# Optimization experiments

Measured on AMD Instinct MI355X. Metric: run time of the kernel, lower is better.

Reference implementation:

```python
import jax, jax.numpy as jnp
import numpy as np

ML_R_PRIORI = 1.5   # mainlobe_window_radius_priori
ML_R_MAX = 4        # mainlobe_window_radius_max
MIN_K = 1           # min_k
ML_WIDTH_POW = 1    # ml_width_pow
DIST_SENTINEL = 100.0


def _grid_offsets(r):
    # all (dy, dx) pairs in [-r, r]^2 -> [(2r+1)^2, 2]
    o = np.arange(-r, r + 1)
    yy, xx = np.meshgrid(o, o, indexing='ij')
    return np.stack([yy.ravel(), xx.ravel()], axis=-1).astype(np.int32)


def setup_inputs() -> dict:
    key = jax.random.key(0)
    B, C, H, W = 256, 324, 18, 18
    k1, k2 = jax.random.split(key)
    cost_volume = jax.random.normal(k1, (B, C, H, W), dtype=jnp.float32)
    peak_coords = jax.random.randint(k2, (B, C, 2), 0, H, dtype=jnp.int32)  # (y, x)
    gy, gx = jnp.meshgrid(jnp.arange(H, dtype=jnp.int32),
                          jnp.arange(W, dtype=jnp.int32), indexing='ij')
    mesh_y = jnp.broadcast_to(gy, (B, C, H, W))
    mesh_x = jnp.broadcast_to(gx, (B, C, H, W))
    return {"cost_volume": cost_volume, "peak_coords": peak_coords,
            "mesh_y": mesh_y, "mesh_x": mesh_x}


def reference(cost_volume, peak_coords, mesh_y, mesh_x):
    B, C, H, W = cost_volume.shape
    BC, HW = B * C, H * W
    cv = cost_volume.reshape(BC, HW)
    peak = peak_coords.reshape(BC, 2)
    my = mesh_y.reshape(BC, HW)
    mx = mesh_x.reshape(BC, HW)

    # --- static offset tables ---
    off_max = jnp.asarray(_grid_offsets(ML_R_MAX))                     # [81, 2]
    off_p = jnp.asarray(_grid_offsets(int(np.ceil(ML_R_PRIORI))))      # [25, 2]
    norm_p = jnp.sqrt(jnp.sum(off_p.astype(jnp.float32) ** 2, -1))
    off_priori = jnp.where((norm_p <= ML_R_PRIORI)[:, None], off_p, 0)  # out-of-radius -> (0,0)

    bidx = jnp.arange(BC)[:, None]

    def scatter_zero_mask(offsets):
        # offsets: [1 or BC, N, 2]; zero out mainlobe window around each peak
        win = peak[:, None, :] + offsets
        wy = jnp.clip(win[..., 0], 0, H - 1)
        wx = jnp.clip(win[..., 1], 0, W - 1)
        flat = wy * W + wx                                  # [BC, N]
        return jnp.ones((BC, HW), jnp.float32).at[bidx, flat].set(0.0)

    # --- priori sidelobe mean ---
    w_pri = scatter_zero_mask(off_priori[None])
    n_pri = w_pri.sum(-1, keepdims=True)
    mean_pri = (cv * w_pri).sum(-1, keepdims=True) / n_pri

    # --- distance to nearest below-mean (sidelobe) point -> mainlobe width ---
    py, px = peak[:, :1], peak[:, 1:]
    dist = jnp.sqrt(((my - py) ** 2 + (mx - px) ** 2).astype(jnp.float32))
    pos = jnp.arange(HW, dtype=jnp.int32)[None]
    peak_flat = py * W + px
    keep = (cv <= mean_pri) & (pos != peak_flat)
    dist = jnp.where(keep, dist, DIST_SENTINEL)
    neg_small, _ = jax.lax.top_k(-dist, MIN_K)              # k smallest distances
    width = (-neg_small).mean(-1, keepdims=True)            # [BC, 1]

    # --- data-dependent mainlobe window (per-row radius) ---
    radius = jnp.clip(width, 1.5, ML_R_MAX + 0.5)           # [BC, 1]
    norms_max = jnp.sqrt(jnp.sum(off_max.astype(jnp.float32) ** 2, -1))  # [81]
    in_r = norms_max[None, :] <= radius                     # [BC, 81]
    off_dyn = jnp.where(in_r[..., None], off_max[None], 0)  # [BC, 81, 2]

    w = scatter_zero_mask(off_dyn)
    n = w.sum(-1, keepdims=True)
    mean_s = (cv * w).sum(-1, keepdims=True) / n
    var_s = (((cv - mean_s) * w) ** 2).sum(-1, keepdims=True) / (n - 1.0)  # use_std_dev=False
    peaks = cv.max(-1, keepdims=True)

    psrw = ((peaks - mean_s) / (var_s * width ** ML_WIDTH_POW + 1e-16)).reshape(B, C)
    saliency = psrw / (psrw.mean(-1, keepdims=True) + 1e-8)
    return saliency
```

## Files before the change

### kernel.cpp

```cpp
#include <hip/hip_runtime.h>
#include <math.h>

constexpr int Hn = 18, Wn = 18, HWn = 324;

__global__ __launch_bounds__(256) void psrw_kernel(
    const float* __restrict__ cv, const int* __restrict__ peak,
    float* __restrict__ out, int BC)
{
    int gtid = blockIdx.x * 256 + threadIdx.x;
    int wave = gtid >> 6;
    int lane = threadIdx.x & 63;
    int g = lane >> 4;
    int l = lane & 15;
    int tile = wave * 4 + g;
    if (tile >= BC) return;

    const float* row = cv + (size_t)tile * HWn;
    int2 pk = ((const int2*)peak)[tile];
    int py = pk.x, px = pk.y;

    const float4* rf4 = (const float4*)row;
    float4 v0 = rf4[l];
    float4 v1 = rf4[l + 16];
    float4 v2 = rf4[l + 32];
    float4 v3 = rf4[l + 48];
    float4 v4 = rf4[l + 64];
    float tl = row[320 + (l & 3)];
    bool valid20 = (l < 4);

    float c[21] = {v0.x, v0.y, v0.z, v0.w, v1.x, v1.y, v1.z, v1.w,
                   v2.x, v2.y, v2.z, v2.w, v3.x, v3.y, v3.z, v3.w,
                   v4.x, v4.y, v4.z, v4.w, valid20 ? tl : 0.f};
    int d2[21];

    float m = -INFINITY, s_pri = 0.f;
    int l4 = 4 * l;
#pragma unroll
    for (int j = 0; j < 21; ++j) {
        int p = (j < 20) ? (l4 + 64 * (j >> 2) + (j & 3)) : (320 + (l & 3));
        int y = (p * 57) >> 10;
        int x = p - 18 * y;
        int dy = y - py, dx = x - px;
        int dd = dy * dy + dx * dx;
        if (j == 20) dd = valid20 ? dd : (1 << 20);
        d2[j] = dd;
        m = fmaxf(m, (j == 20 && !valid20) ? -INFINITY : c[j]);
        s_pri += (dd > 2) ? c[j] : 0.f;
    }
#pragma unroll
    for (int o = 8; o; o >>= 1) {
        s_pri += __shfl_xor(s_pri, o, 64);
        m = fmaxf(m, __shfl_xor(m, o, 64));
    }
    int rh = min(Hn - 1, py + 1) - max(0, py - 1) + 1;
    int rw = min(Wn - 1, px + 1) - max(0, px - 1) + 1;
    int n_pri = HWn - rh * rw;
    float mean_pri = s_pri / (float)n_pri;

    int dmin = 1 << 20;
#pragma unroll
    for (int j = 0; j < 21; ++j) {
        bool keep = (c[j] <= mean_pri) && (d2[j] != 0);
        dmin = min(dmin, keep ? d2[j] : (1 << 20));
    }
#pragma unroll
    for (int o = 8; o; o >>= 1) dmin = min(dmin, __shfl_xor(dmin, o, 64));

    float width = (dmin >= (1 << 20)) ? 100.f : sqrtf((float)dmin);
    int rad2 = (dmin <= 2) ? 2 : ((dmin >= 21) ? 20 : dmin);

    float s_dyn = 0.f, ss_dyn = 0.f;
    int cnt_in = 0;
#pragma unroll
    for (int j = 0; j < 21; ++j) {
        bool in = (d2[j] <= rad2);
        float cm = in ? 0.f : c[j];
        s_dyn += cm;
        ss_dyn = fmaf(cm, cm, ss_dyn);
        cnt_in += in ? 1 : 0;
    }
#pragma unroll
    for (int o = 8; o; o >>= 1) {
        s_dyn  += __shfl_xor(s_dyn, o, 64);
        ss_dyn += __shfl_xor(ss_dyn, o, 64);
        cnt_in += __shfl_xor(cnt_in, o, 64);
    }
    float n = (float)(HWn - cnt_in);
    float mean_s = s_dyn / n;
    float var_s = fmaf(-s_dyn, mean_s, ss_dyn) / (n - 1.f);
    float psrw = (m - mean_s) / fmaf(var_s, width, 1e-16f);
    if (l == 0) out[tile] = psrw;
}

__global__ __launch_bounds__(256) void norm_kernel(float* __restrict__ out, int B)
{
    int gtid = blockIdx.x * 256 + threadIdx.x;
    int wave = gtid >> 6;
    int lane = threadIdx.x & 63;
    if (wave >= B) return;
    float* row = out + (size_t)wave * HWn;
    float4 v0 = reinterpret_cast<float4*>(row)[lane];
    bool has2 = lane < 17;
    float4 v1 = make_float4(0.f, 0.f, 0.f, 0.f);
    if (has2) v1 = reinterpret_cast<float4*>(row)[64 + lane];
    float s = (v0.x + v0.y) + (v0.z + v0.w) + ((v1.x + v1.y) + (v1.z + v1.w));
#pragma unroll
    for (int o = 32; o; o >>= 1) s += __shfl_xor(s, o, 64);
    float denom = s / 324.0f + 1e-8f;
    v0.x /= denom; v0.y /= denom; v0.z /= denom; v0.w /= denom;
    reinterpret_cast<float4*>(row)[lane] = v0;
    if (has2) {
        v1.x /= denom; v1.y /= denom; v1.z /= denom; v1.w /= denom;
        reinterpret_cast<float4*>(row)[64 + lane] = v1;
    }
}

extern "C" void kernel_launch(void* const* d_in, const int* in_sizes, int n_in,
                              void* d_out, int out_size, void* d_ws, size_t ws_size,
                              hipStream_t stream) {
    const float* cv  = (const float*)d_in[0];
    const int* peak  = (const int*)d_in[1];
    float* out = (float*)d_out;

    int BC = in_sizes[1] / 2;
    int waves = (BC + 3) / 4;
    int blocks1 = (waves + 3) / 4;
    psrw_kernel<<<blocks1, 256, 0, stream>>>(cv, peak, out, BC);

    int B = out_size / HWn;
    int blocks2 = (B + 3) / 4;
    norm_kernel<<<blocks2, 256, 0, stream>>>(out, B);
}
```

Baseline: 28.62 us.

## Load columns per lane and compute distances incrementally with unsigned tricks

Each lane now owns one column of the 18x18 tile (scalar strided loads) plus a tail chunk, instead of loading float4 vectors in row-major order. Squared distances are built incrementally from a running quadratic, with the peak excluded by an offset of one. The priori sum subtracts an explicit 3x3 rectangle gathered by lanes, and the peak value is removed by a separate load. Divisions become fast reciprocals, and the peak coordinates are masked with &31. Scalar strided loads replace vectorised loads, which may cost memory efficiency, and the approximate reciprocals slightly change numerics.

```diff
diff --git a/kernel.cpp b/kernel.cpp
--- a/kernel.cpp
+++ b/kernel.cpp
@@ -17,78 +17,107 @@
 
     const float* row = cv + (size_t)tile * HWn;
     int2 pk = ((const int2*)peak)[tile];
-    int py = pk.x, px = pk.y;
+    int py = pk.x & 31, px = pk.y & 31;
 
-    const float4* rf4 = (const float4*)row;
-    float4 v0 = rf4[l];
-    float4 v1 = rf4[l + 16];
-    float4 v2 = rf4[l + 32];
-    float4 v3 = rf4[l + 48];
-    float4 v4 = rf4[l + 64];
-    float tl = row[320 + (l & 3)];
-    bool valid20 = (l < 4);
+    const float* colp = row + l;
+    float c[21];
+#pragma unroll
+    for (int j = 0; j < 18; ++j) c[j] = colp[18 * j];
+    int lh = l >> 1, lb = l & 1;
+    const float* tp = row + (lh * 18 + 16 + lb);
+    c[18] = tp[0];
+    c[19] = tp[144];
+    bool v20 = (l < 4);
+    c[20] = v20 ? tp[288] : 0.f;
 
-    float c[21] = {v0.x, v0.y, v0.z, v0.w, v1.x, v1.y, v1.z, v1.w,
-                   v2.x, v2.y, v2.z, v2.w, v3.x, v3.y, v3.z, v3.w,
-                   v4.x, v4.y, v4.z, v4.w, valid20 ? tl : 0.f};
-    int d2[21];
+    float cpk = row[py * Wn + px];
 
-    float m = -INFINITY, s_pri = 0.f;
-    int l4 = 4 * l;
+    float m0 = -INFINITY, m1 = -INFINITY, s0 = 0.f, s1 = 0.f;
+#pragma unroll
+    for (int j = 0; j < 18; j += 2) { m0 = fmaxf(m0, c[j]); s0 += c[j]; }
+#pragma unroll
+    for (int j = 1; j < 18; j += 2) { m1 = fmaxf(m1, c[j]); s1 += c[j]; }
+    m0 = fmaxf(m0, c[18]); s0 += c[18];
+    m1 = fmaxf(m1, c[19]); s1 += c[19];
+    m0 = fmaxf(m0, v20 ? c[20] : -INFINITY); s0 += c[20];
+    float m = fmaxf(m0, m1);
+    float s = s0 + s1;
+
+    int ry0 = max(0, py - 1), ry1 = min(Hn - 1, py + 1);
+    int rx0 = max(0, px - 1), rx1 = min(Wn - 1, px + 1);
+    float rectc = 0.f;
+    if (l < 9) {
+        int q = (l * 11) >> 5;
+        int r = l - 3 * q;
+        int ry = ry0 + q, rx = rx0 + r;
+        if (ry <= ry1 && rx <= rx1) rectc = row[ry * Wn + rx];
+    }
+    s -= rectc;
+#pragma unroll
+    for (int o = 8; o; o >>= 1) {
+        s += __shfl_xor(s, o, 64);
+        m = fmaxf(m, __shfl_xor(m, o, 64));
+    }
+    int n_pri = HWn - (ry1 - ry0 + 1) * (rx1 - rx0 + 1);
+    float mean_pri = s / (float)n_pri;
+
+    int dxl = l - px;
+    int dx2m1 = dxl * dxl - 1;
+    unsigned ddm1[21];
+    unsigned A = (unsigned)(py * py + dx2m1);
+    int Bstep = 1 - 2 * py;
+    unsigned dminb = 0xFFFFFFFFu;
+#pragma unroll
+    for (int j = 0; j < 18; ++j) {
+        ddm1[j] = A;
+        unsigned t = min(dminb, A);
+        dminb = (c[j] <= mean_pri) ? t : dminb;
+        A += (unsigned)Bstep;
+        Bstep += 2;
+    }
+    int dyt = lh - py;
+    int dxt = 16 + lb - px;
+    int dxt2m1 = dxt * dxt - 1;
+#pragma unroll
+    for (int s2 = 0; s2 < 3; ++s2) {
+        int dy = dyt + 8 * s2;
+        unsigned dd = (unsigned)(dy * dy + dxt2m1);
+        if (s2 == 2 && !v20) dd = 0x7FFFFFFFu;
+        ddm1[18 + s2] = dd;
+        unsigned t = min(dminb, dd);
+        dminb = (c[18 + s2] <= mean_pri) ? t : dminb;
+    }
+#pragma unroll
+    for (int o = 8; o; o >>= 1)
+        dminb = min(dminb, (unsigned)__shfl_xor((int)dminb, o, 64));
+
+    float width = (dminb > 577u) ? 100.f
+                                 : __builtin_amdgcn_sqrtf((float)(dminb + 1u));
+    unsigned rad2m1 = min(max(dminb, 1u), 19u);
+
+    float sd0 = 0.f, sd1 = 0.f, ssd = 0.f;
+    int cnt = 0;
 #pragma unroll
     for (int j = 0; j < 21; ++j) {
-        int p = (j < 20) ? (l4 + 64 * (j >> 2) + (j & 3)) : (320 + (l & 3));
-        int y = (p * 57) >> 10;
-        int x = p - 18 * y;
-        int dy = y - py, dx = x - px;
-        int dd = dy * dy + dx * dx;
-        if (j == 20) dd = valid20 ? dd : (1 << 20);
-        d2[j] = dd;
-        m = fmaxf(m, (j == 20 && !valid20) ? -INFINITY : c[j]);
-        s_pri += (dd > 2) ? c[j] : 0.f;
+        bool in = (ddm1[j] <= rad2m1);
+        float cm = in ? 0.f : c[j];
+        if (j & 1) sd1 += cm; else sd0 += cm;
+        ssd = fmaf(cm, cm, ssd);
+        cnt += in ? 1 : 0;
     }
+    float sd = sd0 + sd1;
 #pragma unroll
     for (int o = 8; o; o >>= 1) {
-        s_pri += __shfl_xor(s_pri, o, 64);
-        m = fmaxf(m, __shfl_xor(m, o, 64));
+        sd  += __shfl_xor(sd, o, 64);
+        ssd += __shfl_xor(ssd, o, 64);
+        cnt += __shfl_xor(cnt, o, 64);
     }
-    int rh = min(Hn - 1, py + 1) - max(0, py - 1) + 1;
-    int rw = min(Wn - 1, px + 1) - max(0, px - 1) + 1;
-    int n_pri = HWn - rh * rw;
-    float mean_pri = s_pri / (float)n_pri;
-
-    int dmin = 1 << 20;
-#pragma unroll
-    for (int j = 0; j < 21; ++j) {
-        bool keep = (c[j] <= mean_pri) && (d2[j] != 0);
-        dmin = min(dmin, keep ? d2[j] : (1 << 20));
-    }
-#pragma unroll
-    for (int o = 8; o; o >>= 1) dmin = min(dmin, __shfl_xor(dmin, o, 64));
-
-    float width = (dmin >= (1 << 20)) ? 100.f : sqrtf((float)dmin);
-    int rad2 = (dmin <= 2) ? 2 : ((dmin >= 21) ? 20 : dmin);
-
-    float s_dyn = 0.f, ss_dyn = 0.f;
-    int cnt_in = 0;
-#pragma unroll
-    for (int j = 0; j < 21; ++j) {
-        bool in = (d2[j] <= rad2);
-        float cm = in ? 0.f : c[j];
-        s_dyn += cm;
-        ss_dyn = fmaf(cm, cm, ss_dyn);
-        cnt_in += in ? 1 : 0;
-    }
-#pragma unroll
-    for (int o = 8; o; o >>= 1) {
-        s_dyn  += __shfl_xor(s_dyn, o, 64);
-        ss_dyn += __shfl_xor(ss_dyn, o, 64);
-        cnt_in += __shfl_xor(cnt_in, o, 64);
-    }
-    float n = (float)(HWn - cnt_in);
-    float mean_s = s_dyn / n;
-    float var_s = fmaf(-s_dyn, mean_s, ss_dyn) / (n - 1.f);
-    float psrw = (m - mean_s) / fmaf(var_s, width, 1e-16f);
+    sd -= cpk;
+    ssd = fmaf(-cpk, cpk, ssd);
+    float n = (float)(HWn - 1 - cnt);
+    float mean_s = sd * __builtin_amdgcn_rcpf(n);
+    float var_s = fmaf(-sd, mean_s, ssd) * __builtin_amdgcn_rcpf(n - 1.f);
+    float psrw = (m - mean_s) * __builtin_amdgcn_rcpf(fmaf(var_s, width, 1e-16f));
     if (l == 0) out[tile] = psrw;
 }
 
```

New measurement: 25.29 us. 1.13x faster.
